# Optimization experiments

Measured on AMD Instinct MI355X. Metric: run time of the kernel, lower is better.

## Reference

```python
import jax, jax.numpy as jnp
import numpy as np

T, B, S, D, H = 1024, 2, 4096, 1024, 16  # queries, batch, kv_len, embed_dim, heads
HD = D // H


def setup_inputs() -> dict:
    key = jax.random.key(0)
    ks = jax.random.split(key, 12)
    f = lambda k, sh: jax.random.normal(k, sh, dtype=jnp.float32)
    w = lambda k: f(k, (D, D)) * 0.02  # torch Linear weight [out, in]
    return {
        "hidden_states": f(ks[0], (T, B, D)),
        "attention_mask": f(ks[1], (B * H, T, S)),
        "position_embeddings": f(ks[2], (T, B, D)),
        "key_value_states": f(ks[3], (S, B, D)),
        "key_value_position_embeddings": f(ks[4], (S, B, D)),
        "Wq": w(ks[5]), "bq": jnp.zeros((D,), jnp.float32),
        "Wk": w(ks[6]), "bk": jnp.zeros((D,), jnp.float32),
        "Wv": w(ks[7]), "bv": jnp.zeros((D,), jnp.float32),
        "Wo": w(ks[8]), "bo": jnp.zeros((D,), jnp.float32),
    }


def reference(hidden_states, attention_mask, position_embeddings,
              key_value_states, key_value_position_embeddings,
              Wq, bq, Wk, bk, Wv, bv, Wo, bo):
    # inputs are [seq, batch, dim]; module permutes to [batch, seq, dim]
    hs = jnp.transpose(hidden_states, (1, 0, 2))            # [B, T, D]
    pos = jnp.transpose(position_embeddings, (1, 0, 2))      # [B, T, D]
    kv = jnp.transpose(key_value_states, (1, 0, 2))          # [B, S, D]
    kvpos = jnp.transpose(key_value_position_embeddings, (1, 0, 2))
    b, t, d = hs.shape
    s = kv.shape[1]
    hd = d // H
    scaling = hd ** -0.5

    q = ((hs + pos) @ Wq.T + bq) * scaling                   # pos-embed added to q
    k = (kv + kvpos) @ Wk.T + bk                             # pos-embed added to k
    v = kv @ Wv.T + bv                                       # v from original kv

    q = q.reshape(b, t, H, hd).transpose(0, 2, 1, 3)         # [B, H, T, hd]
    k = k.reshape(b, s, H, hd).transpose(0, 2, 1, 3)         # [B, H, S, hd]
    v = v.reshape(b, s, H, hd).transpose(0, 2, 1, 3)         # [B, H, S, hd]

    scores = jnp.einsum('bhtd,bhsd->bhts', q, k)             # [B, H, T, S]
    scores = scores + attention_mask.reshape(b, H, t, s)
    probs = jax.nn.softmax(scores, axis=-1)                  # dropout p=0.0 -> identity

    ctx = jnp.einsum('bhts,bhsd->bhtd', probs, v)            # [B, H, T, hd]
    ctx = ctx.transpose(0, 2, 1, 3).reshape(b, t, d)         # [B, T, D]
    out = ctx @ Wo.T + bo
    return jnp.transpose(out, (1, 0, 2))                     # back to [T, B, D]
```

## Files before the change

### kernel.cpp

```cpp
#include <hip/hip_runtime.h>
#include <stdint.h>

typedef __attribute__((ext_vector_type(8))) short short8;
typedef __attribute__((ext_vector_type(4))) float f32x4;
typedef __attribute__((ext_vector_type(4))) unsigned short u16x4;

__device__ __forceinline__ unsigned short f2bf(float x){
  union { float f; unsigned int u; } v; v.f = x;
  unsigned int r = v.u + 0x7fffu + ((v.u >> 16) & 1u);
  return (unsigned short)(r >> 16);
}

__device__ __forceinline__ f32x4 mfma16(short8 a, short8 b, f32x4 c){
  return __builtin_amdgcn_mfma_f32_16x16x32_bf16(a, b, c, 0, 0, 0);
}

__device__ __forceinline__ void async16(const void* g, void* l){
  __builtin_amdgcn_global_load_lds(
      (__attribute__((address_space(1))) void*)g,
      (__attribute__((address_space(3))) void*)l, 16, 0, 0);
}

__global__ __launch_bounds__(256) void k_prep(const float4* __restrict__ a,
                                              const float4* __restrict__ b,
                                              u16x4* __restrict__ o, int n4){
  int i = blockIdx.x * 256 + threadIdx.x;
  if (i >= n4) return;
  float4 x = a[i];
  if (b){ float4 y = b[i]; x.x += y.x; x.y += y.y; x.z += y.z; x.w += y.w; }
  u16x4 r; r.x = f2bf(x.x); r.y = f2bf(x.y); r.z = f2bf(x.z); r.w = f2bf(x.w);
  o[i] = r;
}

template<int MODE>
__global__ __launch_bounds__(256,2) void k_gemm(const unsigned short* __restrict__ A,
    const unsigned short* __restrict__ W, const float* __restrict__ bias,
    void* __restrict__ outp, int M, float scale)
{
  __shared__ unsigned short lA[128*32];
  __shared__ unsigned short lB[128*32];
  const int tid = threadIdx.x, lane = tid & 63, w = tid >> 6;
  const int quad = lane >> 4, m16 = lane & 15;
  const int wm = w & 1, wn = w >> 1;
  const int row0 = blockIdx.x * 128, col0 = blockIdx.y * 128;
  const int g0 = w*64 + lane, g1 = (w+4)*64 + lane;
  const int r0g = g0 & 127, q0g = g0 >> 7;
  const int r1g = g1 & 127, q1g = g1 >> 7;
  const unsigned short* Ab = A + (size_t)row0 * 1024;
  const unsigned short* Bb = W + (size_t)col0 * 1024;
  f32x4 acc[4][4] = {};
  for (int k0 = 0; k0 < 1024; k0 += 32){
    async16(Ab + (size_t)r0g*1024 + k0 + q0g*8, &lA[w*512]);
    async16(Ab + (size_t)r1g*1024 + k0 + q1g*8, &lA[(w+4)*512]);
    async16(Bb + (size_t)r0g*1024 + k0 + q0g*8, &lB[w*512]);
    async16(Bb + (size_t)r1g*1024 + k0 + q1g*8, &lB[(w+4)*512]);
    __syncthreads();
    short8 af[4], bfr[4];
    #pragma unroll
    for (int mt = 0; mt < 4; ++mt)
      af[mt] = *(const short8*)&lA[(quad*128 + wm*64 + mt*16 + m16)*8];
    #pragma unroll
    for (int nt = 0; nt < 4; ++nt)
      bfr[nt] = *(const short8*)&lB[(quad*128 + wn*64 + nt*16 + m16)*8];
    #pragma unroll
    for (int mt = 0; mt < 4; ++mt)
      #pragma unroll
      for (int nt = 0; nt < 4; ++nt)
        acc[mt][nt] = mfma16(af[mt], bfr[nt], acc[mt][nt]);
    __syncthreads();
  }
  if (MODE == 0){
    unsigned short* out16 = (unsigned short*)outp;
    const int SEQ = M >> 1;
    #pragma unroll
    for (int nt = 0; nt < 4; ++nt){
      const int n = col0 + wn*64 + nt*16 + m16;
      const float bvv = bias[n];
      const int h = n >> 6, d = n & 63;
      #pragma unroll
      for (int mt = 0; mt < 4; ++mt){
        const int rbase = row0 + wm*64 + mt*16 + quad*4;
        #pragma unroll
        for (int r = 0; r < 4; ++r){
          const int rr = rbase + r;
          const int seq = rr >> 1, bb = rr & 1;
          const float vv = (acc[mt][nt][r] + bvv) * scale;
          out16[(((size_t)(bb*16 + h) * SEQ + seq) << 6) + d] = f2bf(vv);
        }
      }
    }
  } else {
    float* outf = (float*)outp;
    #pragma unroll
    for (int nt = 0; nt < 4; ++nt){
      const int n = col0 + wn*64 + nt*16 + m16;
      const float bvv = bias[n];
      #pragma unroll
      for (int mt = 0; mt < 4; ++mt){
        const int rbase = row0 + wm*64 + mt*16 + quad*4;
        #pragma unroll
        for (int r = 0; r < 4; ++r){
          const int rr = rbase + r;
          const int tt = rr & 1023, bb = rr >> 10;
          outf[(((size_t)tt*2 + bb) << 10) + n] = acc[mt][nt][r] + bvv;
        }
      }
    }
  }
}

__global__ __launch_bounds__(256) void k_tr(const unsigned short* __restrict__ V,
                                            unsigned short* __restrict__ VT){
  __shared__ unsigned short t[64*73];
  const int tid = threadIdx.x;
  const int bh = blockIdx.x >> 6;
  const int s0 = (blockIdx.x & 63) << 6;
  #pragma unroll
  for (int j = 0; j < 2; ++j){
    int g = j*256 + tid;
    int s = g >> 3, d0 = (g & 7)*8;
    short8 x = *(const short8*)&V[(((size_t)bh*4096 + s0 + s) << 6) + d0];
    #pragma unroll
    for (int k = 0; k < 8; ++k)
      t[(d0 + k)*73 + s] = (unsigned short)x[k];
  }
  __syncthreads();
  #pragma unroll
  for (int j = 0; j < 2; ++j){
    int g = j*256 + tid;
    int d = g >> 3, sc = (g & 7)*8;
    short8 r;
    #pragma unroll
    for (int k = 0; k < 8; ++k)
      r[k] = (short)t[d*73 + sc + k];
    *(short8*)&VT[(((size_t)bh*64 + d) << 12) + s0 + sc] = r;
  }
}

__global__ __launch_bounds__(256,2) void k_flash(const unsigned short* __restrict__ Qp,
    const unsigned short* __restrict__ Kp, const unsigned short* __restrict__ VTp,
    const float* __restrict__ mask, unsigned short* __restrict__ ctx)
{
  __shared__ unsigned short pl[4096];
  const int tid = threadIdx.x, lane = tid & 63, w = tid >> 6;
  const int quad = lane >> 4, m16 = lane & 15;
  const int bh = blockIdx.x >> 4;
  const int t0 = ((blockIdx.x & 15) << 6) + w*16;
  short8 qa0, qa1;
  {
    const unsigned short* qp = Qp + (((size_t)bh*1024 + t0 + m16) << 6) + quad*8;
    qa0 = *(const short8*)qp;
    qa1 = *(const short8*)(qp + 32);
  }
  const unsigned short* kb = Kp + (((size_t)bh*4096 + m16) << 6) + quad*8;
  const unsigned short* vb = VTp + (((size_t)(bh*64 + m16)) << 12) + quad*8;
  const float* mb = mask + ((size_t)bh*1024 + t0 + quad*4) * 4096 + m16;
  unsigned short* pw = &pl[w*1024];
  const unsigned short* prd0 = &pl[w*1024 + (quad*16 + m16)*8];
  const unsigned short* prd1 = &pl[w*1024 + ((quad+4)*16 + m16)*8];
  const int pwbase = (m16 >> 3)*128 + quad*32 + (m16 & 7);
  f32x4 Oa[4] = {};
  float mrow[4], lrow[4];
  #pragma unroll
  for (int r = 0; r < 4; ++r){ mrow[r] = -1e30f; lrow[r] = 0.f; }
  const f32x4 zero4 = {0.f, 0.f, 0.f, 0.f};
  for (int s0 = 0; s0 < 4096; s0 += 64){
    f32x4 sc[4];
    #pragma unroll
    for (int c = 0; c < 4; ++c){
      const unsigned short* kp = kb + ((size_t)(s0 + c*16) << 6);
      short8 kf0 = *(const short8*)kp;
      short8 kf1 = *(const short8*)(kp + 32);
      f32x4 z = mfma16(qa0, kf0, zero4);
      sc[c] = mfma16(qa1, kf1, z);
    }
    const float* mp = mb + s0;
    #pragma unroll
    for (int c = 0; c < 4; ++c)
      #pragma unroll
      for (int r = 0; r < 4; ++r)
        sc[c][r] += __builtin_nontemporal_load(mp + (size_t)r*4096 + c*16);
    float rmax[4];
    #pragma unroll
    for (int r = 0; r < 4; ++r)
      rmax[r] = fmaxf(fmaxf(sc[0][r], sc[1][r]), fmaxf(sc[2][r], sc[3][r]));
    #pragma unroll
    for (int off = 1; off <= 8; off <<= 1)
      #pragma unroll
      for (int r = 0; r < 4; ++r)
        rmax[r] = fmaxf(rmax[r], __shfl_xor(rmax[r], off, 64));
    float al[4], rsum[4];
    #pragma unroll
    for (int r = 0; r < 4; ++r){
      float mn = fmaxf(mrow[r], rmax[r]);
      al[r] = __expf(mrow[r] - mn);
      mrow[r] = mn;
      rsum[r] = 0.f;
    }
    #pragma unroll
    for (int c = 0; c < 4; ++c)
      #pragma unroll
      for (int r = 0; r < 4; ++r){
        float p = __expf(sc[c][r] - mrow[r]);
        sc[c][r] = p;
        rsum[r] += p;
      }
    #pragma unroll
    for (int off = 1; off <= 8; off <<= 1)
      #pragma unroll
      for (int r = 0; r < 4; ++r)
        rsum[r] += __shfl_xor(rsum[r], off, 64);
    #pragma unroll
    for (int r = 0; r < 4; ++r)
      lrow[r] = lrow[r]*al[r] + rsum[r];
    #pragma unroll
    for (int cn = 0; cn < 4; ++cn)
      #pragma unroll
      for (int r = 0; r < 4; ++r)
        Oa[cn][r] *= al[r];
    #pragma unroll
    for (int c = 0; c < 4; ++c)
      #pragma unroll
      for (int r = 0; r < 4; ++r)
        pw[pwbase + c*256 + r*8] = f2bf(sc[c][r]);
    asm volatile("s_waitcnt lgkmcnt(0)" ::: "memory");
    short8 pa0 = *(const short8*)prd0;
    short8 pa1 = *(const short8*)prd1;
    #pragma unroll
    for (int cn = 0; cn < 4; ++cn){
      const unsigned short* vp = vb + ((size_t)cn << 16) + s0;
      short8 v0 = *(const short8*)vp;
      short8 v1 = *(const short8*)(vp + 32);
      Oa[cn] = mfma16(pa0, v0, Oa[cn]);
      Oa[cn] = mfma16(pa1, v1, Oa[cn]);
    }
  }
  const int b = bh >> 4, h = bh & 15;
  unsigned short* op = ctx + (((size_t)b*1024 + t0 + quad*4) << 10) + h*64 + m16;
  #pragma unroll
  for (int r = 0; r < 4; ++r){
    float inv = 1.f / lrow[r];
    #pragma unroll
    for (int cn = 0; cn < 4; ++cn)
      op[((size_t)r << 10) + cn*16] = f2bf(Oa[cn][r]*inv);
  }
}

extern "C" void kernel_launch(void* const* d_in, const int* in_sizes, int n_in,
                              void* d_out, int out_size, void* d_ws, size_t ws_size,
                              hipStream_t stream)
{
  (void)in_sizes; (void)n_in; (void)out_size; (void)ws_size;
  const float* hs    = (const float*)d_in[0];
  const float* mask  = (const float*)d_in[1];
  const float* pos   = (const float*)d_in[2];
  const float* kv    = (const float*)d_in[3];
  const float* kvpos = (const float*)d_in[4];
  const float* Wq = (const float*)d_in[5];  const float* biq = (const float*)d_in[6];
  const float* Wk = (const float*)d_in[7];  const float* bik = (const float*)d_in[8];
  const float* Wv = (const float*)d_in[9];  const float* biv = (const float*)d_in[10];
  const float* Wo = (const float*)d_in[11]; const float* bio = (const float*)d_in[12];
  float* out = (float*)d_out;
  char* ws = (char*)d_ws;
  unsigned short* Aq  = (unsigned short*)(ws + ( 0ull << 20));
  unsigned short* Ak  = (unsigned short*)(ws + ( 4ull << 20));
  unsigned short* Av  = (unsigned short*)(ws + (20ull << 20));
  unsigned short* Wqb = (unsigned short*)(ws + (36ull << 20));
  unsigned short* Wkb = (unsigned short*)(ws + (38ull << 20));
  unsigned short* Wvb = (unsigned short*)(ws + (40ull << 20));
  unsigned short* Wob = (unsigned short*)(ws + (42ull << 20));
  unsigned short* Qb  = (unsigned short*)(ws + (44ull << 20));
  unsigned short* Kb  = (unsigned short*)(ws + (48ull << 20));
  unsigned short* Vb  = (unsigned short*)(ws + ( 4ull << 20));
  unsigned short* VTb = (unsigned short*)(ws + (20ull << 20));
  unsigned short* ctx = (unsigned short*)(ws + (36ull << 20));

  k_prep<<<dim3(2048), dim3(256), 0, stream>>>((const float4*)hs, (const float4*)pos,
                                               (u16x4*)Aq, 524288);
  k_prep<<<dim3(8192), dim3(256), 0, stream>>>((const float4*)kv, (const float4*)kvpos,
                                               (u16x4*)Ak, 2097152);
  k_prep<<<dim3(8192), dim3(256), 0, stream>>>((const float4*)kv, nullptr,
                                               (u16x4*)Av, 2097152);
  k_prep<<<dim3(1024), dim3(256), 0, stream>>>((const float4*)Wq, nullptr,
                                               (u16x4*)Wqb, 262144);
  k_prep<<<dim3(1024), dim3(256), 0, stream>>>((const float4*)Wk, nullptr,
                                               (u16x4*)Wkb, 262144);
  k_prep<<<dim3(1024), dim3(256), 0, stream>>>((const float4*)Wv, nullptr,
                                               (u16x4*)Wvb, 262144);
  k_prep<<<dim3(1024), dim3(256), 0, stream>>>((const float4*)Wo, nullptr,
                                               (u16x4*)Wob, 262144);

  k_gemm<0><<<dim3(16, 8), dim3(256), 0, stream>>>(Aq, Wqb, biq, Qb, 2048, 0.125f);
  k_gemm<0><<<dim3(64, 8), dim3(256), 0, stream>>>(Ak, Wkb, bik, Kb, 8192, 1.0f);
  k_gemm<0><<<dim3(64, 8), dim3(256), 0, stream>>>(Av, Wvb, biv, Vb, 8192, 1.0f);
  k_tr<<<dim3(2048), dim3(256), 0, stream>>>(Vb, VTb);
  k_flash<<<dim3(512), dim3(256), 0, stream>>>(Qb, Kb, VTb, mask, ctx);
  k_gemm<1><<<dim3(16, 8), dim3(256), 0, stream>>>(ctx, Wob, bio, out, 2048, 1.0f);
}
```

Measured before the change: 1.069 ms.

## Fuse prep kernels, write V transposed from GEMM, double-buffer flash loads

Seven fp32-to-bf16 conversion launches become one kernel that also reads kv once to produce both K and V inputs. The V projection GEMM now writes its result directly in transposed layout, which removes the separate transpose kernel and its extra round trip through memory. The flash kernel prefetches the K fragments and mask values for the next 64-key tile into registers while the current tile is processed, and loads V before the softmax. It also applies an XOR swizzle to the P tile in LDS to cut bank conflicts. The costs are higher register pressure in the flash kernel and scattered, uncoalesced stores from the transposed V epilogue.

```diff
diff --git a/kernel.cpp b/kernel.cpp
--- a/kernel.cpp
+++ b/kernel.cpp
@@ -21,15 +21,40 @@
       (__attribute__((address_space(3))) void*)l, 16, 0, 0);
 }
 
-__global__ __launch_bounds__(256) void k_prep(const float4* __restrict__ a,
-                                              const float4* __restrict__ b,
-                                              u16x4* __restrict__ o, int n4){
+__device__ __forceinline__ u16x4 cvt4(float4 x){
+  u16x4 r; r.x = f2bf(x.x); r.y = f2bf(x.y); r.z = f2bf(x.z); r.w = f2bf(x.w);
+  return r;
+}
+
+__global__ __launch_bounds__(256) void k_prep_all(
+    const float4* __restrict__ hs, const float4* __restrict__ pos,
+    const float4* __restrict__ kv, const float4* __restrict__ kvpos,
+    const float4* __restrict__ Wq, const float4* __restrict__ Wk,
+    const float4* __restrict__ Wv, const float4* __restrict__ Wo,
+    u16x4* __restrict__ Aq, u16x4* __restrict__ Ak, u16x4* __restrict__ Av,
+    u16x4* __restrict__ Wqb, u16x4* __restrict__ Wkb,
+    u16x4* __restrict__ Wvb, u16x4* __restrict__ Wob)
+{
   int i = blockIdx.x * 256 + threadIdx.x;
-  if (i >= n4) return;
-  float4 x = a[i];
-  if (b){ float4 y = b[i]; x.x += y.x; x.y += y.y; x.z += y.z; x.w += y.w; }
-  u16x4 r; r.x = f2bf(x.x); r.y = f2bf(x.y); r.z = f2bf(x.z); r.w = f2bf(x.w);
-  o[i] = r;
+  if (i < 524288){
+    float4 a = hs[i], b = pos[i];
+    a.x += b.x; a.y += b.y; a.z += b.z; a.w += b.w;
+    Aq[i] = cvt4(a);
+  } else if (i < 2621440){
+    int j = i - 524288;
+    float4 a = kv[j], b = kvpos[j];
+    Av[j] = cvt4(a);
+    a.x += b.x; a.y += b.y; a.z += b.z; a.w += b.w;
+    Ak[j] = cvt4(a);
+  } else if (i < 2883584){
+    int j = i - 2621440; Wqb[j] = cvt4(Wq[j]);
+  } else if (i < 3145728){
+    int j = i - 2883584; Wkb[j] = cvt4(Wk[j]);
+  } else if (i < 3407872){
+    int j = i - 3145728; Wvb[j] = cvt4(Wv[j]);
+  } else {
+    int j = i - 3407872; Wob[j] = cvt4(Wo[j]);
+  }
 }
 
 template<int MODE>
@@ -89,7 +114,7 @@
         }
       }
     }
-  } else {
+  } else if (MODE == 1){
     float* outf = (float*)outp;
     #pragma unroll
     for (int nt = 0; nt < 4; ++nt){
@@ -106,34 +131,24 @@
         }
       }
     }
-  }
-}
-
-__global__ __launch_bounds__(256) void k_tr(const unsigned short* __restrict__ V,
-                                            unsigned short* __restrict__ VT){
-  __shared__ unsigned short t[64*73];
-  const int tid = threadIdx.x;
-  const int bh = blockIdx.x >> 6;
-  const int s0 = (blockIdx.x & 63) << 6;
-  #pragma unroll
-  for (int j = 0; j < 2; ++j){
-    int g = j*256 + tid;
-    int s = g >> 3, d0 = (g & 7)*8;
-    short8 x = *(const short8*)&V[(((size_t)bh*4096 + s0 + s) << 6) + d0];
-    #pragma unroll
-    for (int k = 0; k < 8; ++k)
-      t[(d0 + k)*73 + s] = (unsigned short)x[k];
-  }
-  __syncthreads();
-  #pragma unroll
-  for (int j = 0; j < 2; ++j){
-    int g = j*256 + tid;
-    int d = g >> 3, sc = (g & 7)*8;
-    short8 r;
-    #pragma unroll
-    for (int k = 0; k < 8; ++k)
-      r[k] = (short)t[d*73 + sc + k];
-    *(short8*)&VT[(((size_t)bh*64 + d) << 12) + s0 + sc] = r;
+  } else {
+    unsigned short* out16 = (unsigned short*)outp;
+    #pragma unroll
+    for (int nt = 0; nt < 4; ++nt){
+      const int n = col0 + wn*64 + nt*16 + m16;
+      const float bvv = bias[n];
+      const int h = n >> 6, d = n & 63;
+      #pragma unroll
+      for (int mt = 0; mt < 4; ++mt){
+        const int rbase = row0 + wm*64 + mt*16 + quad*4;
+        #pragma unroll
+        for (int r = 0; r < 4; ++r){
+          const int rr = rbase + r;
+          const int seq = rr >> 1, bb = rr & 1;
+          out16[(((size_t)((bb*16 + h)*64 + d)) << 12) + seq] = f2bf(acc[mt][nt][r] + bvv);
+        }
+      }
+    }
   }
 }
 
@@ -156,30 +171,52 @@
   const unsigned short* vb = VTp + (((size_t)(bh*64 + m16)) << 12) + quad*8;
   const float* mb = mask + ((size_t)bh*1024 + t0 + quad*4) * 4096 + m16;
   unsigned short* pw = &pl[w*1024];
-  const unsigned short* prd0 = &pl[w*1024 + (quad*16 + m16)*8];
-  const unsigned short* prd1 = &pl[w*1024 + ((quad+4)*16 + m16)*8];
-  const int pwbase = (m16 >> 3)*128 + quad*32 + (m16 & 7);
+  const unsigned short* prd0 = &pl[w*1024 + (quad*16 + (m16 ^ quad))*8];
+  const unsigned short* prd1 = &pl[w*1024 + ((quad+4)*16 + (m16 ^ (quad+4)))*8];
   f32x4 Oa[4] = {};
   float mrow[4], lrow[4];
   #pragma unroll
   for (int r = 0; r < 4; ++r){ mrow[r] = -1e30f; lrow[r] = 0.f; }
   const f32x4 zero4 = {0.f, 0.f, 0.f, 0.f};
-  for (int s0 = 0; s0 < 4096; s0 += 64){
-    f32x4 sc[4];
+
+  short8 kA[8], kB[8];
+  float mA[16], mB[16];
+
+  auto LK = [&](int s0, short8* kf){
     #pragma unroll
     for (int c = 0; c < 4; ++c){
       const unsigned short* kp = kb + ((size_t)(s0 + c*16) << 6);
-      short8 kf0 = *(const short8*)kp;
-      short8 kf1 = *(const short8*)(kp + 32);
-      f32x4 z = mfma16(qa0, kf0, zero4);
-      sc[c] = mfma16(qa1, kf1, z);
-    }
+      kf[2*c]   = *(const short8*)kp;
+      kf[2*c+1] = *(const short8*)(kp + 32);
+    }
+  };
+  auto LM = [&](int s0, float* mf){
     const float* mp = mb + s0;
     #pragma unroll
     for (int c = 0; c < 4; ++c)
       #pragma unroll
       for (int r = 0; r < 4; ++r)
-        sc[c][r] += __builtin_nontemporal_load(mp + (size_t)r*4096 + c*16);
+        mf[c*4+r] = __builtin_nontemporal_load(mp + (size_t)r*4096 + c*16);
+  };
+  auto PROC = [&](int s0, const short8* kf, const float* mf){
+    f32x4 sc[4];
+    #pragma unroll
+    for (int c = 0; c < 4; ++c){
+      f32x4 z = mfma16(qa0, kf[2*c], zero4);
+      sc[c] = mfma16(qa1, kf[2*c+1], z);
+    }
+    short8 vf[8];
+    #pragma unroll
+    for (int cn = 0; cn < 4; ++cn){
+      const unsigned short* vp = vb + ((size_t)cn << 16) + s0;
+      vf[2*cn]   = *(const short8*)vp;
+      vf[2*cn+1] = *(const short8*)(vp + 32);
+    }
+    #pragma unroll
+    for (int c = 0; c < 4; ++c)
+      #pragma unroll
+      for (int r = 0; r < 4; ++r)
+        sc[c][r] += mf[c*4+r];
     float rmax[4];
     #pragma unroll
     for (int r = 0; r < 4; ++r)
@@ -219,22 +256,32 @@
       for (int r = 0; r < 4; ++r)
         Oa[cn][r] *= al[r];
     #pragma unroll
-    for (int c = 0; c < 4; ++c)
-      #pragma unroll
-      for (int r = 0; r < 4; ++r)
-        pw[pwbase + c*256 + r*8] = f2bf(sc[c][r]);
+    for (int c = 0; c < 4; ++c){
+      const int kch = c*2 + (m16 >> 3);
+      #pragma unroll
+      for (int r = 0; r < 4; ++r){
+        const int row = quad*4 + r;
+        pw[(kch*16 + (row ^ kch))*8 + (m16 & 7)] = f2bf(sc[c][r]);
+      }
+    }
     asm volatile("s_waitcnt lgkmcnt(0)" ::: "memory");
     short8 pa0 = *(const short8*)prd0;
     short8 pa1 = *(const short8*)prd1;
     #pragma unroll
     for (int cn = 0; cn < 4; ++cn){
-      const unsigned short* vp = vb + ((size_t)cn << 16) + s0;
-      short8 v0 = *(const short8*)vp;
-      short8 v1 = *(const short8*)(vp + 32);
-      Oa[cn] = mfma16(pa0, v0, Oa[cn]);
-      Oa[cn] = mfma16(pa1, v1, Oa[cn]);
-    }
-  }
+      Oa[cn] = mfma16(pa0, vf[2*cn], Oa[cn]);
+      Oa[cn] = mfma16(pa1, vf[2*cn+1], Oa[cn]);
+    }
+  };
+
+  LK(0, kA); LM(0, mA);
+  for (int s0 = 0; s0 < 4096; s0 += 128){
+    LK(s0+64, kB); LM(s0+64, mB);
+    PROC(s0, kA, mA);
+    if (s0 + 128 < 4096){ LK(s0+128, kA); LM(s0+128, mA); }
+    PROC(s0+64, kB, mB);
+  }
+
   const int b = bh >> 4, h = bh & 15;
   unsigned short* op = ctx + (((size_t)b*1024 + t0 + quad*4) << 10) + h*64 + m16;
   #pragma unroll
@@ -271,29 +318,18 @@
   unsigned short* Wob = (unsigned short*)(ws + (42ull << 20));
   unsigned short* Qb  = (unsigned short*)(ws + (44ull << 20));
   unsigned short* Kb  = (unsigned short*)(ws + (48ull << 20));
-  unsigned short* Vb  = (unsigned short*)(ws + ( 4ull << 20));
-  unsigned short* VTb = (unsigned short*)(ws + (20ull << 20));
+  unsigned short* VTb = (unsigned short*)(ws + (64ull << 20));
   unsigned short* ctx = (unsigned short*)(ws + (36ull << 20));
 
-  k_prep<<<dim3(2048), dim3(256), 0, stream>>>((const float4*)hs, (const float4*)pos,
-                                               (u16x4*)Aq, 524288);
-  k_prep<<<dim3(8192), dim3(256), 0, stream>>>((const float4*)kv, (const float4*)kvpos,
-                                               (u16x4*)Ak, 2097152);
-  k_prep<<<dim3(8192), dim3(256), 0, stream>>>((const float4*)kv, nullptr,
-                                               (u16x4*)Av, 2097152);
-  k_prep<<<dim3(1024), dim3(256), 0, stream>>>((const float4*)Wq, nullptr,
-                                               (u16x4*)Wqb, 262144);
-  k_prep<<<dim3(1024), dim3(256), 0, stream>>>((const float4*)Wk, nullptr,
-                                               (u16x4*)Wkb, 262144);
-  k_prep<<<dim3(1024), dim3(256), 0, stream>>>((const float4*)Wv, nullptr,
-                                               (u16x4*)Wvb, 262144);
-  k_prep<<<dim3(1024), dim3(256), 0, stream>>>((const float4*)Wo, nullptr,
-                                               (u16x4*)Wob, 262144);
+  k_prep_all<<<dim3(14336), dim3(256), 0, stream>>>(
+      (const float4*)hs, (const float4*)pos, (const float4*)kv, (const float4*)kvpos,
+      (const float4*)Wq, (const float4*)Wk, (const float4*)Wv, (const float4*)Wo,
+      (u16x4*)Aq, (u16x4*)Ak, (u16x4*)Av,
+      (u16x4*)Wqb, (u16x4*)Wkb, (u16x4*)Wvb, (u16x4*)Wob);
 
   k_gemm<0><<<dim3(16, 8), dim3(256), 0, stream>>>(Aq, Wqb, biq, Qb, 2048, 0.125f);
   k_gemm<0><<<dim3(64, 8), dim3(256), 0, stream>>>(Ak, Wkb, bik, Kb, 8192, 1.0f);
-  k_gemm<0><<<dim3(64, 8), dim3(256), 0, stream>>>(Av, Wvb, biv, Vb, 8192, 1.0f);
-  k_tr<<<dim3(2048), dim3(256), 0, stream>>>(Vb, VTb);
+  k_gemm<2><<<dim3(64, 8), dim3(256), 0, stream>>>(Av, Wvb, biv, VTb, 8192, 1.0f);
   k_flash<<<dim3(512), dim3(256), 0, stream>>>(Qb, Kb, VTb, mask, ctx);
   k_gemm<1><<<dim3(16, 8), dim3(256), 0, stream>>>(ctx, Wob, bio, out, 2048, 1.0f);
 }
```

Result: no change. 1.052 ms (-1.6%).
